# Kernel optimization log

Measured on AMD Instinct MI355X. Metric: run time of the kernel, lower is better.

The kernel has to match this reference:

```python
import jax, jax.numpy as jnp
import numpy as np

N_P, N_W, F_IN = 512, 3584, 256
H1, O1 = 8, 32
H2, O2 = 8, 256
BATCH = 1024
NEG_SLOPE = 0.2


def _xavier(key, shape):
    fan_in, fan_out = shape[-2], shape[-1]
    lim = jnp.sqrt(6.0 / (fan_in + fan_out))
    return jax.random.uniform(key, shape, jnp.float32, -lim, lim)


def setup_inputs() -> dict:
    key = jax.random.key(0)
    ks = jax.random.split(key, 16)
    return {
        "input": jax.random.uniform(ks[0], (BATCH, N_W), jnp.float32),
        "pern_feature": jax.random.normal(ks[1], (N_P, F_IN), jnp.float32),
        "word_feature": jax.random.normal(ks[2], (N_W, F_IN), jnp.float32),
        "w1": _xavier(ks[3], (H1, F_IN, O1)),
        "a_src1": _xavier(ks[4], (H1, O1, 1)),
        "a_dst1": _xavier(ks[5], (H1, O1, 1)),
        "b1": jnp.zeros((O1,), jnp.float32),
        "w2": _xavier(ks[6], (H2, F_IN, O2)),
        "a_src2": _xavier(ks[7], (H2, F_IN, 1)),
        "a_dst2": _xavier(ks[8], (H2, F_IN, 1)),
        "b2": jnp.zeros((O2,), jnp.float32),
        "W_fc": _xavier(ks[9], (O2, 5)),
        "b_fc": jnp.zeros((5,), jnp.float32),
        "pern_adj": jax.random.randint(ks[10], (N_P, N_P), 0, 2, jnp.int32),
        "word_pern_adj": jax.random.randint(ks[11], (N_P + N_W, N_P + N_W), 0, 2, jnp.int32),
    }


def gat(h, adj, w, a_src, a_dst, bias):
    # h: [N, f_in], adj: [N, N] int, w: [H, f_in, f_out]
    h_prime = jnp.einsum('nf,hfo->hno', h, w)          # [H, N, O]
    t = jnp.tanh(h_prime)
    s_src = jnp.einsum('hno,hoi->hn', t, a_src)        # [H, N]
    s_dst = jnp.einsum('hno,hoi->hn', t, a_dst)        # [H, N]
    attn = s_src[:, :, None] + s_dst[:, None, :]       # [H, N, N]
    attn = jnp.where(attn >= 0, attn, NEG_SLOPE * attn)  # leaky_relu
    attn = jnp.where(adj[None, :, :] > 0, attn, -jnp.inf)
    attn = jax.nn.softmax(attn, axis=-1)
    out = jnp.einsum('hnm,hmo->hno', attn, h_prime)    # [H, N, O]
    return out + bias


def reference(input, pern_feature, word_feature, w1, a_src1, a_dst1, b1,
              w2, a_src2, a_dst2, b2, W_fc, b_fc, pern_adj, word_pern_adj):
    n_p = pern_feature.shape[0]
    # GAT 1 over personality graph
    h1 = gat(pern_feature, pern_adj, w1, a_src1, a_dst1, b1)       # [H1, n_p, O1]
    hiddn_pp = jnp.transpose(h1, (1, 0, 2)).reshape(n_p, -1)        # [n_p, H1*O1]
    hiddn_pp = jax.nn.elu(hiddn_pp)
    # dropout is identity in eval mode
    hiddn_wp = jnp.concatenate([word_feature, hiddn_pp], axis=0)    # [N, 256]
    h2 = gat(hiddn_wp, word_pern_adj, w2, a_src2, a_dst2, b2)       # [H2, N, O2]
    hiddn_wp2 = h2.mean(axis=0)                                     # [N, O2]
    hiddn_w = hiddn_wp2[:word_feature.shape[0], :]                  # [n_w, O2]
    x = (input @ hiddn_w) / input.sum(axis=1, keepdims=True)        # [B, O2]
    return x @ W_fc + b_fc                                          # [B, 5]
```

## Files before the change

### kernel.cpp

```cpp
#include <hip/hip_runtime.h>
#include <hip/hip_bf16.h>
#include <math.h>

#define NP 512
#define NW 3584
#define NT 4096
#define FIN 256
#define H1 8
#define O1 32
#define H2 8
#define O2 256
#define NEG 0.2f

typedef __attribute__((ext_vector_type(8))) short bf16x8;
typedef __attribute__((ext_vector_type(4))) float f32x4;
typedef __attribute__((ext_vector_type(2))) float v2f;
typedef unsigned long long u64;

__device__ __forceinline__ unsigned short f2bf(float f) {
    unsigned u = __float_as_uint(f);
    unsigned r = (u + 0x7FFF + ((u >> 16) & 1)) >> 16;
    return (unsigned short)r;
}

__device__ __forceinline__ float fast_tanh(float x) {
    float ex = __expf(2.0f * x);
    return 1.0f - 2.0f / (ex + 1.0f);
}

__global__ __launch_bounds__(256) void k_prep(
    const float* __restrict__ wf, const float* __restrict__ pf,
    const float* __restrict__ w1, const float* __restrict__ a_src1,
    const float* __restrict__ a_dst1, const float* __restrict__ w2,
    const float* __restrict__ b2, const float* __restrict__ W_fc,
    const int* __restrict__ wp_adj,
    unsigned short* __restrict__ abf, unsigned short* __restrict__ btbf,
    float* __restrict__ hp1, float* __restrict__ ss1, float* __restrict__ sd1,
    unsigned* __restrict__ maskT, float* __restrict__ cvec)
{
    __shared__ float tile[64][65];
    __shared__ float feat[2][FIN];
    __shared__ float red[4][5];
    int blk = blockIdx.x;
    int t = threadIdx.x;
    if (blk < 896) {
        int idx4 = blk * 256 + t;
        float4 x = ((const float4*)wf)[idx4];
        ushort4 y;
        y.x = f2bf(x.x); y.y = f2bf(x.y); y.z = f2bf(x.z); y.w = f2bf(x.w);
        ((ushort4*)abf)[idx4] = y;
    } else if (blk < 1152) {
        int n0 = (blk - 896) * 2;
        feat[0][t] = pf[n0 * FIN + t];
        feat[1][t] = pf[(n0 + 1) * FIN + t];
        __syncthreads();
        int h = t >> 5, o = t & 31;
        float acc0 = 0.f, acc1 = 0.f;
        const float* wcol = w1 + h * FIN * O1 + o;
        #pragma unroll 4
        for (int f = 0; f < FIN; f++) {
            float w = wcol[f * O1];
            acc0 += feat[0][f] * w;
            acc1 += feat[1][f] * w;
        }
        hp1[n0 * 256 + t] = acc0;
        hp1[(n0 + 1) * 256 + t] = acc1;
        float as = a_src1[h * O1 + o];
        float ad = a_dst1[h * O1 + o];
        float accs[2] = {acc0, acc1};
        #pragma unroll
        for (int i = 0; i < 2; i++) {
            float th = tanhf(accs[i]);
            float vs = th * as, vd = th * ad;
            #pragma unroll
            for (int off = 1; off < 32; off <<= 1) {
                vs += __shfl_xor(vs, off);
                vd += __shfl_xor(vd, off);
            }
            if (o == 0) { ss1[h * NP + n0 + i] = vs; sd1[h * NP + n0 + i] = vd; }
        }
    } else if (blk < 1280) {
        int blk2 = blk - 1152;
        int h = blk2 >> 4;
        int f0 = ((blk2 >> 2) & 3) * 64;
        int o0 = (blk2 & 3) * 64;
        #pragma unroll
        for (int rr = 0; rr < 16; rr++) {
            int f = rr * 4 + (t >> 6);
            int o = t & 63;
            tile[f][o] = w2[((size_t)(h * FIN + f0 + f)) * O2 + o0 + o];
        }
        __syncthreads();
        #pragma unroll
        for (int rr = 0; rr < 16; rr++) {
            int o = rr * 4 + (t >> 6);
            int f = t & 63;
            btbf[((size_t)(h * O2 + o0 + o)) * FIN + f0 + f] = f2bf(tile[f][o]);
        }
    } else if (blk < 2176) {
        int w = t >> 6, l = t & 63;
        int r = (blk - 1280) * 4 + w;
        const int4* row = (const int4*)(wp_adj + (size_t)r * NT);
        for (int c4 = 0; c4 < 16; c4++) {
            int4 x = row[c4 * 64 + l];
            u64 nib = (u64)((x.x != 0 ? 1 : 0) | (x.y != 0 ? 2 : 0) |
                            (x.z != 0 ? 4 : 0) | (x.w != 0 ? 8 : 0));
            u64 v = nib << (4 * (l & 15));
            v |= __shfl_xor(v, 1);
            v |= __shfl_xor(v, 2);
            v |= __shfl_xor(v, 4);
            v |= __shfl_xor(v, 8);
            if ((l & 15) == 0) {
                int qw = c4 * 4 + (l >> 4);
                maskT[(size_t)(2 * qw) * NW + r]     = (unsigned)v;
                maskT[(size_t)(2 * qw + 1) * NW + r] = (unsigned)(v >> 32);
            }
        }
    } else {
        float v[5];
        #pragma unroll
        for (int j = 0; j < 5; j++) v[j] = b2[t] * W_fc[t * 5 + j];
        #pragma unroll
        for (int off = 1; off < 64; off <<= 1)
            #pragma unroll
            for (int j = 0; j < 5; j++) v[j] += __shfl_xor(v[j], off);
        int w = t >> 6, l = t & 63;
        if (l == 0) { for (int j = 0; j < 5; j++) red[w][j] = v[j]; }
        __syncthreads();
        if (t == 0)
            for (int j = 0; j < 5; j++) cvec[j] = red[0][j] + red[1][j] + red[2][j] + red[3][j];
    }
}

__global__ __launch_bounds__(256) void k_gat1_attn(
    const int* __restrict__ adj, const float* __restrict__ hp1,
    const float* __restrict__ ss1, const float* __restrict__ sd1,
    const float* __restrict__ b1, unsigned short* __restrict__ abf)
{
    __shared__ float p[2][H1][NP];
    __shared__ float den[2][H1];
    int t = threadIdx.x;
    int n0 = blockIdx.x * 2;
    for (int rr = 0; rr < 32; rr++) {
        int idx = rr * 256 + t;
        int i = idx >> 12, h = (idx >> 9) & 7, m = idx & 511;
        float a = adj[(n0 + i) * NP + m] > 0 ? 1.0f : 0.0f;
        float e = ss1[h * NP + n0 + i] + sd1[h * NP + m];
        e = fmaxf(e, NEG * e);
        p[i][h][m] = a * __expf(e);
    }
    __syncthreads();
    int w = t >> 6, l = t & 63;
    {
        int i = w & 1;
        #pragma unroll
        for (int hh = 0; hh < 4; hh++) {
            int h = (w >> 1) * 4 + hh;
            float s = 0;
            #pragma unroll
            for (int q = 0; q < 8; q++) s += p[i][h][l + 64 * q];
            #pragma unroll
            for (int off = 1; off < 64; off <<= 1) s += __shfl_xor(s, off);
            if (l == 0) den[i][h] = s;
        }
    }
    __syncthreads();
    int h = t >> 5, o = t & 31;
    float acc[2] = {0, 0};
    #pragma unroll 4
    for (int m = 0; m < NP; m++) {
        float v = hp1[m * 256 + t];
        acc[0] += p[0][h][m] * v;
        acc[1] += p[1][h][m] * v;
    }
    float bo = b1[o];
    #pragma unroll
    for (int i = 0; i < 2; i++) {
        float r = acc[i] / den[i][h] + bo;
        r = r > 0.f ? r : expm1f(r);
        abf[(NW + n0 + i) * FIN + t] = f2bf(r);
    }
}

__global__ __launch_bounds__(256) void k_gemm_hp2(
    const unsigned short* __restrict__ abf, const unsigned short* __restrict__ btbf,
    const float* __restrict__ a_src2, const float* __restrict__ a_dst2,
    const float* __restrict__ W_fc, float* __restrict__ gpart)
{
    int bid = blockIdx.x;
    int h = bid >> 6;
    int rem = bid & 63;
    int mt = rem >> 1, nt = rem & 1;
    int w = threadIdx.x >> 6, l = threadIdx.x & 63;
    int m0 = mt * 128 + (w >> 1) * 64;
    int n0 = nt * 128 + (w & 1) * 64;
    int lr = l & 15, lq = l >> 4;
    const unsigned short* bbase = btbf + h * O2 * FIN;
    f32x4 acc[4][4];
    #pragma unroll
    for (int i = 0; i < 4; i++)
        #pragma unroll
        for (int j = 0; j < 4; j++) acc[i][j] = (f32x4){0.f, 0.f, 0.f, 0.f};
    for (int k = 0; k < FIN; k += 32) {
        bf16x8 a[4], b[4];
        int kc = k + lq * 8;
        #pragma unroll
        for (int i = 0; i < 4; i++)
            a[i] = *(const bf16x8*)(abf + (m0 + i * 16 + lr) * FIN + kc);
        #pragma unroll
        for (int j = 0; j < 4; j++)
            b[j] = *(const bf16x8*)(bbase + (n0 + j * 16 + lr) * FIN + kc);
        #pragma unroll
        for (int i = 0; i < 4; i++)
            #pragma unroll
            for (int j = 0; j < 4; j++)
                acc[i][j] = __builtin_amdgcn_mfma_f32_16x16x32_bf16(a[i], b[j], acc[i][j], 0, 0, 0);
    }
    int slice = nt * 2 + (w & 1);
    float as[4], ad[4], wfc[4][5];
    #pragma unroll
    for (int j = 0; j < 4; j++) {
        int col = n0 + j * 16 + lr;
        as[j] = a_src2[h * O2 + col];
        ad[j] = a_dst2[h * O2 + col];
        #pragma unroll
        for (int jj = 0; jj < 5; jj++) wfc[j][jj] = W_fc[col * 5 + jj];
    }
    float* base = gpart + ((size_t)h * 4 + slice) * NT * 8;
    #pragma unroll
    for (int i = 0; i < 4; i++) {
        #pragma unroll
        for (int r = 0; r < 4; r++) {
            float s[7] = {0,0,0,0,0,0,0};
            #pragma unroll
            for (int j = 0; j < 4; j++) {
                float x = acc[i][j][r];
                float th = fast_tanh(x);
                s[0] += th * as[j];
                s[1] += th * ad[j];
                #pragma unroll
                for (int jj = 0; jj < 5; jj++) s[2 + jj] += x * wfc[j][jj];
            }
            #pragma unroll
            for (int off = 1; off < 16; off <<= 1)
                #pragma unroll
                for (int q = 0; q < 7; q++) s[q] += __shfl_xor(s[q], off);
            if (lr == 0) {
                int m = m0 + i * 16 + lq * 4 + r;
                float* dst = base + (size_t)m * 8;
                #pragma unroll
                for (int q = 0; q < 7; q++) dst[q] = s[q];
            }
        }
    }
}

__global__ __launch_bounds__(256) void k_comb_hp2(
    const float* __restrict__ gpart,
    float* __restrict__ Etab, float* __restrict__ Eptab, float* __restrict__ T)
{
    int idx = blockIdx.x * 256 + threadIdx.x;
    float s[7] = {0,0,0,0,0,0,0};
    #pragma unroll
    for (int sl = 0; sl < 4; sl++) {
        const float* p = gpart + (((size_t)(idx >> 12) * 4 + sl) * NT + (idx & (NT - 1))) * 8;
        #pragma unroll
        for (int q = 0; q < 7; q++) s[q] += p[q];
    }
    Etab[idx]  = __expf(s[0]);
    Eptab[idx] = __expf(NEG * s[0]);
    float4 t0 = {__expf(s[1]), __expf(NEG * s[1]), 1.0f, s[2]};
    float4 t1 = {s[3], s[4], s[5], s[6]};
    *(float4*)(T + (size_t)idx * 8)     = t0;
    *(float4*)(T + (size_t)idx * 8 + 4) = t1;
}

__global__ __launch_bounds__(512, 4) void k_gat2_attn(
    const unsigned* __restrict__ maskT, const float* __restrict__ Etab,
    const float* __restrict__ Eptab, const float* __restrict__ T,
    float* __restrict__ part)
{
    __shared__ unsigned pw[64 * 64];
    int t = threadIdx.x;
    int w = t >> 6, l = t & 63;
    int b = blockIdx.x;
    int nb = b % 56;
    int h  = (b / 56) & 7;
    int c  = b / 448;
    int rbase = nb * 64;
    #pragma unroll
    for (int u = 0; u < 8; u++) {
        int idx = u * 512 + t;
        int wd = idx >> 6, row = idx & 63;
        pw[idx] = maskT[(size_t)(c * 64 + wd) * NW + rbase + row];
    }
    __syncthreads();
    int n0 = rbase + w * 8;
    u64 epk[8];
    #pragma unroll
    for (int i = 0; i < 8; i++) {
        int r = h * NT + n0 + i;
        unsigned e  = __builtin_amdgcn_readfirstlane(__float_as_uint(Etab[r]));
        unsigned ep = __builtin_amdgcn_readfirstlane(__float_as_uint(Eptab[r]));
        epk[i] = ((u64)ep << 32) | e;
    }
    v2f accA[8], accB[8], accC[8];
    #pragma unroll
    for (int i = 0; i < 8; i++) {
        accA[i] = (v2f){0.f, 0.f}; accB[i] = (v2f){0.f, 0.f}; accC[i] = (v2f){0.f, 0.f};
    }
    const float* Th = T + ((size_t)h * NT + c * 2048) * 8;
    const unsigned* mbase = pw + (l >> 5) * 64 + w * 8;
    int lsh = l & 31;
    for (int q = 0; q < 32; q++) {
        const float* tp = Th + (size_t)(q * 64 + l) * 8;
        f32x4 t0 = *(const f32x4*)tp;
        f32x4 t1 = *(const f32x4*)(tp + 4);
        v2f ffp = {t0.x, t0.y};
        v2f g01 = {t0.z, t0.w};
        v2f g12 = {t1.x, t1.y};
        v2f g34 = {t1.z, t1.w};
        uint4 ma = *(const uint4*)(mbase + q * 128);
        uint4 mb = *(const uint4*)(mbase + q * 128 + 4);
        unsigned wv[8] = {ma.x, ma.y, ma.z, ma.w, mb.x, mb.y, mb.z, mb.w};
        #pragma unroll
        for (int i = 0; i < 8; i++) {
            float bm = (float)((wv[i] >> lsh) & 1u);
            v2f pab;
            asm("v_pk_mul_f32 %0, %1, %2" : "=v"(pab) : "v"(ffp), "s"(epk[i]));
            float pp = fmaxf(pab.x, pab.y) * bm;
            v2f ppv; ppv.x = pp; ppv.y = pp;
            asm("v_pk_fma_f32 %0, %1, %2, %0" : "+v"(accA[i]) : "v"(ppv), "v"(g01));
            asm("v_pk_fma_f32 %0, %1, %2, %0" : "+v"(accB[i]) : "v"(ppv), "v"(g12));
            asm("v_pk_fma_f32 %0, %1, %2, %0" : "+v"(accC[i]) : "v"(ppv), "v"(g34));
        }
    }
    #pragma unroll
    for (int i = 0; i < 8; i++) {
        float v[6];
        v[0] = accA[i].x; v[1] = accA[i].y;
        v[2] = accB[i].x; v[3] = accB[i].y;
        v[4] = accC[i].x; v[5] = accC[i].y;
        #pragma unroll
        for (int off = 1; off < 8; off <<= 1)
            #pragma unroll
            for (int k = 0; k < 6; k++) v[k] += __shfl_xor(v[k], off);
        if ((l & 7) == 0) {
            float* dst = part + ((((size_t)c * NW + n0 + i) * 8 + h) * 8 + (l >> 3)) * 8;
            #pragma unroll
            for (int k = 0; k < 6; k++) dst[k] = v[k];
        }
    }
}

__global__ __launch_bounds__(256) void k_gat2_comb(const float* __restrict__ part,
                                                   float* __restrict__ hf) {
    int idx = blockIdx.x * 256 + threadIdx.x;
    int n = idx >> 3, h = idx & 7;
    float den = 0, num[5] = {0,0,0,0,0};
    #pragma unroll
    for (int cc = 0; cc < 2; cc++) {
        #pragma unroll
        for (int s = 0; s < 8; s++) {
            const float* p = part + ((((size_t)cc * NW + n) * 8 + h) * 8 + s) * 8;
            float4 a = *(const float4*)p;
            float4 bq = *(const float4*)(p + 4);
            den += a.x;
            num[0] += a.y; num[1] += a.z; num[2] += a.w;
            num[3] += bq.x; num[4] += bq.y;
        }
    }
    float inv = 1.0f / (den * 8.0f);
    float v[5];
    #pragma unroll
    for (int j = 0; j < 5; j++) v[j] = num[j] * inv;
    #pragma unroll
    for (int off = 1; off < 8; off <<= 1)
        #pragma unroll
        for (int j = 0; j < 5; j++) v[j] += __shfl_xor(v[j], off);
    if (h == 0) {
        #pragma unroll
        for (int j = 0; j < 5; j++) hf[n * 5 + j] = v[j];
    }
}

__global__ __launch_bounds__(256) void k_final(
    const float* __restrict__ input, const float* __restrict__ hf,
    const float* __restrict__ cvec, const float* __restrict__ b_fc,
    float* __restrict__ out)
{
    int b = blockIdx.x, t = threadIdx.x;
    const float4* row4 = (const float4*)(input + (size_t)b * NW);
    const float4* hf4 = (const float4*)hf;
    float s = 0.f, a[5] = {0.f, 0.f, 0.f, 0.f, 0.f};
    for (int idx = t; idx < NW / 4; idx += 256) {
        float4 x = row4[idx];
        float f[20];
        #pragma unroll
        for (int q = 0; q < 5; q++) *(float4*)(f + 4 * q) = hf4[idx * 5 + q];
        s += x.x + x.y + x.z + x.w;
        #pragma unroll
        for (int j = 0; j < 5; j++)
            a[j] += x.x * f[j] + x.y * f[5 + j] + x.z * f[10 + j] + x.w * f[15 + j];
    }
    #pragma unroll
    for (int off = 1; off < 64; off <<= 1) {
        s += __shfl_xor(s, off);
        #pragma unroll
        for (int j = 0; j < 5; j++) a[j] += __shfl_xor(a[j], off);
    }
    __shared__ float red[4][6];
    int w = t >> 6, l = t & 63;
    if (l == 0) { red[w][0] = s; for (int j = 0; j < 5; j++) red[w][j + 1] = a[j]; }
    __syncthreads();
    if (t < 5) {
        float st = red[0][0] + red[1][0] + red[2][0] + red[3][0];
        float aj = red[0][t + 1] + red[1][t + 1] + red[2][t + 1] + red[3][t + 1];
        out[b * 5 + t] = aj / st + cvec[t] + b_fc[t];
    }
}

extern "C" void kernel_launch(void* const* d_in, const int* in_sizes, int n_in,
                              void* d_out, int out_size, void* d_ws, size_t ws_size,
                              hipStream_t stream) {
    const float* input   = (const float*)d_in[0];
    const float* pf      = (const float*)d_in[1];
    const float* wf      = (const float*)d_in[2];
    const float* w1      = (const float*)d_in[3];
    const float* a_src1  = (const float*)d_in[4];
    const float* a_dst1  = (const float*)d_in[5];
    const float* b1      = (const float*)d_in[6];
    const float* w2      = (const float*)d_in[7];
    const float* a_src2  = (const float*)d_in[8];
    const float* a_dst2  = (const float*)d_in[9];
    const float* b2      = (const float*)d_in[10];
    const float* W_fc    = (const float*)d_in[11];
    const float* b_fc    = (const float*)d_in[12];
    const int* pern_adj  = (const int*)d_in[13];
    const int* wp_adj    = (const int*)d_in[14];
    float* out = (float*)d_out;

    char* ws = (char*)d_ws;
    unsigned short* abf    = (unsigned short*)(ws);
    unsigned short* btbf   = (unsigned short*)(ws + 2097152);
    float*          hp1    = (float*)(ws + 3145728);
    float*          ss1    = (float*)(ws + 3670016);
    float*          sd1    = (float*)(ws + 3686400);
    float*          Etab   = (float*)(ws + 3833856);
    float*          Eptab  = (float*)(ws + 3964928);
    float*          T      = (float*)(ws + 4096000);
    float*          hf     = (float*)(ws + 5144576);
    float*          cvec   = (float*)(ws + 5216256);
    unsigned*       maskT  = (unsigned*)(ws + 5216512);
    float*          gpart  = (float*)(ws + 7051520);
    float*          part   = (float*)(ws + 11245824);

    k_prep<<<2177, 256, 0, stream>>>(wf, pf, w1, a_src1, a_dst1, w2, b2, W_fc,
                                     wp_adj, abf, btbf, hp1, ss1, sd1, maskT, cvec);
    k_gat1_attn<<<256, 256, 0, stream>>>(pern_adj, hp1, ss1, sd1, b1, abf);
    k_gemm_hp2<<<512, 256, 0, stream>>>(abf, btbf, a_src2, a_dst2, W_fc, gpart);
    k_comb_hp2<<<128, 256, 0, stream>>>(gpart, Etab, Eptab, T);
    k_gat2_attn<<<896, 512, 0, stream>>>(maskT, Etab, Eptab, T, part);
    k_gat2_comb<<<112, 256, 0, stream>>>(part, hf);
    k_final<<<1024, 256, 0, stream>>>(input, hf, cvec, b_fc, out);
}
```

Measured before the change: 281.9 us.

## Use 64-bit mask words as scalar lane masks in GAT2 attention kernel

```diff
diff --git a/kernel.cpp b/kernel.cpp
--- a/kernel.cpp
+++ b/kernel.cpp
@@ -36,7 +36,7 @@
     const int* __restrict__ wp_adj,
     unsigned short* __restrict__ abf, unsigned short* __restrict__ btbf,
     float* __restrict__ hp1, float* __restrict__ ss1, float* __restrict__ sd1,
-    unsigned* __restrict__ maskT, float* __restrict__ cvec)
+    u64* __restrict__ maskT64, float* __restrict__ cvec)
 {
     __shared__ float tile[64][65];
     __shared__ float feat[2][FIN];
@@ -112,8 +112,7 @@
             v |= __shfl_xor(v, 8);
             if ((l & 15) == 0) {
                 int qw = c4 * 4 + (l >> 4);
-                maskT[(size_t)(2 * qw) * NW + r]     = (unsigned)v;
-                maskT[(size_t)(2 * qw + 1) * NW + r] = (unsigned)(v >> 32);
+                maskT64[(size_t)qw * NW + r] = v;
             }
         }
     } else {
@@ -275,27 +274,18 @@
     *(float4*)(T + (size_t)idx * 8 + 4) = t1;
 }
 
-__global__ __launch_bounds__(512, 4) void k_gat2_attn(
-    const unsigned* __restrict__ maskT, const float* __restrict__ Etab,
+__global__ __launch_bounds__(256) void k_gat2_attn(
+    const u64* __restrict__ maskT64, const float* __restrict__ Etab,
     const float* __restrict__ Eptab, const float* __restrict__ T,
     float* __restrict__ part)
 {
-    __shared__ unsigned pw[64 * 64];
     int t = threadIdx.x;
     int w = t >> 6, l = t & 63;
     int b = blockIdx.x;
-    int nb = b % 56;
-    int h  = (b / 56) & 7;
-    int c  = b / 448;
-    int rbase = nb * 64;
-    #pragma unroll
-    for (int u = 0; u < 8; u++) {
-        int idx = u * 512 + t;
-        int wd = idx >> 6, row = idx & 63;
-        pw[idx] = maskT[(size_t)(c * 64 + wd) * NW + rbase + row];
-    }
-    __syncthreads();
-    int n0 = rbase + w * 8;
+    int nb = b % 112;
+    int h  = (b / 112) & 7;
+    int c  = b / 896;
+    int n0 = __builtin_amdgcn_readfirstlane(nb * 32 + w * 8);
     u64 epk[8];
     #pragma unroll
     for (int i = 0; i < 8; i++) {
@@ -304,43 +294,41 @@
         unsigned ep = __builtin_amdgcn_readfirstlane(__float_as_uint(Eptab[r]));
         epk[i] = ((u64)ep << 32) | e;
     }
-    v2f accA[8], accB[8], accC[8];
-    #pragma unroll
-    for (int i = 0; i < 8; i++) {
-        accA[i] = (v2f){0.f, 0.f}; accB[i] = (v2f){0.f, 0.f}; accC[i] = (v2f){0.f, 0.f};
-    }
+    float den[8] = {0,0,0,0,0,0,0,0};
+    float num[8][5] = {{0}};
     const float* Th = T + ((size_t)h * NT + c * 2048) * 8;
-    const unsigned* mbase = pw + (l >> 5) * 64 + w * 8;
-    int lsh = l & 31;
     for (int q = 0; q < 32; q++) {
         const float* tp = Th + (size_t)(q * 64 + l) * 8;
         f32x4 t0 = *(const f32x4*)tp;
         f32x4 t1 = *(const f32x4*)(tp + 4);
         v2f ffp = {t0.x, t0.y};
-        v2f g01 = {t0.z, t0.w};
-        v2f g12 = {t1.x, t1.y};
-        v2f g34 = {t1.z, t1.w};
-        uint4 ma = *(const uint4*)(mbase + q * 128);
-        uint4 mb = *(const uint4*)(mbase + q * 128 + 4);
-        unsigned wv[8] = {ma.x, ma.y, ma.z, ma.w, mb.x, mb.y, mb.z, mb.w};
+        size_t moff = (size_t)(c * 32 + q) * NW + n0;
+        const u64* mq = maskT64 + moff;
         #pragma unroll
         for (int i = 0; i < 8; i++) {
-            float bm = (float)((wv[i] >> lsh) & 1u);
+            u64 wv = mq[i];
+            unsigned wlo = __builtin_amdgcn_readfirstlane((unsigned)wv);
+            unsigned whi = __builtin_amdgcn_readfirstlane((unsigned)(wv >> 32));
+            u64 word = ((u64)whi << 32) | wlo;
             v2f pab;
             asm("v_pk_mul_f32 %0, %1, %2" : "=v"(pab) : "v"(ffp), "s"(epk[i]));
-            float pp = fmaxf(pab.x, pab.y) * bm;
-            v2f ppv; ppv.x = pp; ppv.y = pp;
-            asm("v_pk_fma_f32 %0, %1, %2, %0" : "+v"(accA[i]) : "v"(ppv), "v"(g01));
-            asm("v_pk_fma_f32 %0, %1, %2, %0" : "+v"(accB[i]) : "v"(ppv), "v"(g12));
-            asm("v_pk_fma_f32 %0, %1, %2, %0" : "+v"(accC[i]) : "v"(ppv), "v"(g34));
+            float pp0 = fmaxf(pab.x, pab.y);
+            float pp;
+            asm("v_cndmask_b32 %0, 0, %1, %2" : "=v"(pp) : "v"(pp0), "s"(word));
+            den[i] += pp;
+            num[i][0] = fmaf(pp, t0.w, num[i][0]);
+            num[i][1] = fmaf(pp, t1.x, num[i][1]);
+            num[i][2] = fmaf(pp, t1.y, num[i][2]);
+            num[i][3] = fmaf(pp, t1.z, num[i][3]);
+            num[i][4] = fmaf(pp, t1.w, num[i][4]);
         }
     }
     #pragma unroll
     for (int i = 0; i < 8; i++) {
         float v[6];
-        v[0] = accA[i].x; v[1] = accA[i].y;
-        v[2] = accB[i].x; v[3] = accB[i].y;
-        v[4] = accC[i].x; v[5] = accC[i].y;
+        v[0] = den[i];
+        #pragma unroll
+        for (int j = 0; j < 5; j++) v[1 + j] = num[i][j];
         #pragma unroll
         for (int off = 1; off < 8; off <<= 1)
             #pragma unroll
@@ -451,16 +439,16 @@
     float*          T      = (float*)(ws + 4096000);
     float*          hf     = (float*)(ws + 5144576);
     float*          cvec   = (float*)(ws + 5216256);
-    unsigned*       maskT  = (unsigned*)(ws + 5216512);
+    u64*            maskT64= (u64*)(ws + 5216512);
     float*          gpart  = (float*)(ws + 7051520);
     float*          part   = (float*)(ws + 11245824);
 
     k_prep<<<2177, 256, 0, stream>>>(wf, pf, w1, a_src1, a_dst1, w2, b2, W_fc,
-                                     wp_adj, abf, btbf, hp1, ss1, sd1, maskT, cvec);
+                                     wp_adj, abf, btbf, hp1, ss1, sd1, maskT64, cvec);
     k_gat1_attn<<<256, 256, 0, stream>>>(pern_adj, hp1, ss1, sd1, b1, abf);
     k_gemm_hp2<<<512, 256, 0, stream>>>(abf, btbf, a_src2, a_dst2, W_fc, gpart);
     k_comb_hp2<<<128, 256, 0, stream>>>(gpart, Etab, Eptab, T);
-    k_gat2_attn<<<896, 512, 0, stream>>>(maskT, Etab, Eptab, T, part);
+    k_gat2_attn<<<1792, 256, 0, stream>>>(maskT64, Etab, Eptab, T, part);
     k_gat2_comb<<<112, 256, 0, stream>>>(part, hf);
     k_final<<<1024, 256, 0, stream>>>(input, hf, cvec, b_fc, out);
 }
```

Measured after the change: 274.4 us. -2.6%, faster.
